# Kernel tuning notes

Hardware: AMD Instinct MI355X
Metric: run time of the kernel (lower is better)

## Reference

```python
import jax, jax.numpy as jnp
import numpy as np

B, T, DIM = 4, 1024, 2048
H, KVH = 16, 4
HD = DIM // H          # 128
G = H // KVH           # GQA group size = 4


def setup_inputs() -> dict:
    key = jax.random.key(0)
    ks = jax.random.split(key, 4)
    s = 1.0 / np.sqrt(DIM)
    x = jax.random.normal(ks[0], (B, T, DIM), jnp.float32)
    Wq = jax.random.normal(ks[1], (DIM, DIM), jnp.float32) * s
    Wkv = jax.random.normal(ks[2], (DIM, 2 * KVH * HD), jnp.float32) * s
    Wo = jax.random.normal(ks[3], (DIM, DIM), jnp.float32) * s
    # RoPE tables (theta=10000, half-split / rotate-half convention)
    inv_freq = 1.0 / (10000.0 ** (np.arange(0, HD, 2, dtype=np.float64) / HD))
    freqs = np.outer(np.arange(T, dtype=np.float64), inv_freq)  # [T, HD/2]
    cos = jnp.asarray(np.cos(freqs), jnp.float32)
    sin = jnp.asarray(np.sin(freqs), jnp.float32)
    return {"x": x, "Wq": Wq, "Wkv": Wkv, "Wo": Wo, "cos": cos, "sin": sin}


def _rope(u, cos, sin):
    # u: [B,T,heads,HD]; cos/sin: [T, HD/2]
    u1, u2 = jnp.split(u, 2, axis=-1)
    c = cos[None, :, None, :]
    s = sin[None, :, None, :]
    return jnp.concatenate([u1 * c - u2 * s, u1 * s + u2 * c], axis=-1)


def reference(x, Wq, Wkv, Wo, cos, sin):
    Bs, Ts, C = x.shape
    q = (x @ Wq).reshape(Bs, Ts, H, HD)
    kv = (x @ Wkv).reshape(Bs, Ts, 2, KVH, HD)
    k, v = kv[:, :, 0], kv[:, :, 1]
    q = _rope(q, cos, sin)
    k = _rope(k, cos, sin)
    # GQA without materializing repeated K/V: fold group dim into q
    qg = q.reshape(Bs, Ts, KVH, G, HD)
    scores = jnp.einsum('bqhgd,bkhd->bhgqk', qg, k) / np.float32(np.sqrt(HD))
    causal = jnp.tril(jnp.ones((Ts, Ts), bool))
    neg = jnp.finfo(scores.dtype).min
    scores = jnp.where(causal, scores, neg)
    att = jax.nn.softmax(scores, axis=-1)
    out = jnp.einsum('bhgqk,bkhd->bqhgd', att, v).reshape(Bs, Ts, C)
    return out @ Wo
```

## Files before the change

kernel.cpp:

```cpp
#include <hip/hip_runtime.h>

typedef unsigned short u16;
typedef unsigned int u32;
typedef __bf16 bf16x8 __attribute__((ext_vector_type(8)));
typedef float f32x4 __attribute__((ext_vector_type(4)));

#define BB   4
#define TT   1024
#define CDIM 2048
#define NH   16
#define NKV  4
#define HDIM 128

__device__ __forceinline__ float b2f(u16 u) {
    union { u32 i; float f; } x; x.i = ((u32)u) << 16; return x.f;
}
__device__ __forceinline__ u16 f2b(float f) {
    union { float f; u32 i; } x; x.f = f;
    u32 r = (x.i + 0x7fffu + ((x.i >> 16) & 1u)) >> 16;
    return (u16)r;
}
__device__ __forceinline__ void async16(const void* g, void* l) {
    __builtin_amdgcn_global_load_lds((const __attribute__((address_space(1))) void*)g,
                                     (__attribute__((address_space(3))) void*)l, 16, 0, 0);
}
template<int N> __device__ __forceinline__ void waitvm() {
    static_assert(N >= 0 && N <= 8, "unsupported vmcnt");
    if constexpr (N == 0)      asm volatile("s_waitcnt vmcnt(0)" ::: "memory");
    else if constexpr (N == 1) asm volatile("s_waitcnt vmcnt(1)" ::: "memory");
    else if constexpr (N == 2) asm volatile("s_waitcnt vmcnt(2)" ::: "memory");
    else if constexpr (N == 3) asm volatile("s_waitcnt vmcnt(3)" ::: "memory");
    else if constexpr (N == 4) asm volatile("s_waitcnt vmcnt(4)" ::: "memory");
    else if constexpr (N == 5) asm volatile("s_waitcnt vmcnt(5)" ::: "memory");
    else if constexpr (N == 6) asm volatile("s_waitcnt vmcnt(6)" ::: "memory");
    else if constexpr (N == 7) asm volatile("s_waitcnt vmcnt(7)" ::: "memory");
    else                       asm volatile("s_waitcnt vmcnt(8)" ::: "memory");
}

__device__ __forceinline__ bool wave_is_f32(const u16* xp) {
    u16 v = xp[(threadIdx.x & 63) * 2];
    int e = (v >> 7) & 0xFF;
    bool bad = (v != 0) && (e < 90 || e > 160);
    return __popcll(__ballot(bad)) > 16;
}

__global__ __launch_bounds__(256) void pre_k(const void* __restrict__ x,
                                             const void* __restrict__ Wq,
                                             const void* __restrict__ Wkv,
                                             const void* __restrict__ Wo,
                                             u16* __restrict__ xb,
                                             u16* __restrict__ csb,
                                             u16* __restrict__ snb,
                                             u16* __restrict__ WqkvT,
                                             u16* __restrict__ WoT,
                                             const void* __restrict__ cs,
                                             const void* __restrict__ sn) {
    const bool f32m = wave_is_f32((const u16*)x);
    int bid = blockIdx.x;
    if (bid < 8320) {
        const void* src; u16* dst; int i;
        if (bid < 8192)      { src = x;  dst = xb;  i = bid * 256 + threadIdx.x; }
        else if (bid < 8256) { src = cs; dst = csb; i = (bid - 8192) * 256 + threadIdx.x; }
        else                 { src = sn; dst = snb; i = (bid - 8256) * 256 + threadIdx.x; }
        union { u16 u[4]; ushort4 v; } o;
        if (f32m) {
            float4 f = ((const float4*)src)[i];
            o.u[0] = f2b(f.x); o.u[1] = f2b(f.y); o.u[2] = f2b(f.z); o.u[3] = f2b(f.w);
        } else {
            o.v = ((const ushort4*)src)[i];
        }
        ((ushort4*)dst)[i] = o.v;
        return;
    }
    __shared__ alignas(16) u16 tile[64 * 65];
    int t = bid - 8320;
    const void* W; u16* WT; int rows, cols, bx, by;
    if (t < 1024)      { W = Wq;  WT = WqkvT;                    rows = 2048; cols = 2048; bx = t & 31;  by = t >> 5; }
    else if (t < 1536) { int l = t - 1024; W = Wkv; WT = WqkvT + (long)2048 * 2048; rows = 2048; cols = 1024; bx = l & 15; by = l >> 4; }
    else               { int l = t - 1536; W = Wo;  WT = WoT;  rows = 2048; cols = 2048; bx = l & 31;   by = l >> 5; }
    const int r0 = by * 64, c0 = bx * 64;
#pragma unroll
    for (int i = 0; i < 16; i++) {
        int c = threadIdx.x + i * 256;
        int rr = c >> 6, cc = c & 63;
        long idx = (long)(r0 + rr) * cols + c0 + cc;
        tile[rr * 65 + cc] = f32m ? f2b(((const float*)W)[idx]) : ((const u16*)W)[idx];
    }
    __syncthreads();
#pragma unroll
    for (int i = 0; i < 16; i++) {
        int c = threadIdx.x + i * 256;
        int rr = c >> 6, cc = c & 63;
        WT[(long)(c0 + rr) * rows + r0 + cc] = tile[cc * 65 + rr];
    }
}

template<int BM, int BN>
__global__ __launch_bounds__(512, 2) void gemm_p4(const u16* __restrict__ A,
                                                  const u16* __restrict__ Bt,
                                                  void* __restrict__ C,
                                                  int N, int Kd,
                                                  const u16* __restrict__ xprobe) {
    constexpr int MF  = BM / 32;
    constexpr int NF  = BN / 64;
    constexpr int MF0 = MF / 2, MF1 = MF - MF0;
    constexpr int NF0 = (NF + 1) / 2, NF1 = NF - NF0;
    constexpr int NAU = BM / 64;
    constexpr int NBU = BN / 64;
    constexpr int NAL = NAU / 2;
    constexpr int NBL = NBU / 2;

    __shared__ alignas(16) u16 As[2][BM * 64];
    __shared__ alignas(16) u16 Bs[2][BN * 64];

    const bool f32m = (xprobe != nullptr) && wave_is_f32(xprobe);
    const int tid = threadIdx.x;
    const int w = tid >> 6, lane = tid & 63;
    const int wm = w >> 2, wn = w & 3;
    const int l16 = lane & 15, quad = lane >> 4;
    const long arow0 = (long)blockIdx.y * BM;
    const long brow0 = (long)blockIdx.x * BN;
    const int NT = Kd >> 6;

    const int srow = tid >> 3, scp = tid & 7;
    const long gst = (long)srow * Kd + ((scp ^ (srow & 7)) << 3);
    const int cst = tid << 3;

    const u16* Ab = A + arow0 * Kd;
    const u16* Bb = Bt + brow0 * Kd;

    auto stageA = [&](int buf, int t, int u0, int u1) {
#pragma unroll
        for (int u = 0; u < NAU; u++)
            if (u >= u0 && u < u1)
                async16(Ab + (long)u * 64 * Kd + t * 64 + gst, &As[buf][u * 4096 + cst]);
    };
    auto stageB = [&](int buf, int t, int u0, int u1) {
#pragma unroll
        for (int u = 0; u < NBU; u++)
            if (u >= u0 && u < u1)
                async16(Bb + (long)u * 64 * Kd + t * 64 + gst, &Bs[buf][u * 4096 + cst]);
    };

    const int R0a = wm * (BM / 2) + l16, sA = R0a & 7;
    const int R0b = wn * (BN / 4) + l16, sB = R0b & 7;
    int aoff[2], boff[2];
    aoff[0] = R0a * 64 + ((quad ^ sA) << 3);
    aoff[1] = R0a * 64 + (((4 + quad) ^ sA) << 3);
    boff[0] = R0b * 64 + ((quad ^ sB) << 3);
    boff[1] = R0b * 64 + (((4 + quad) ^ sB) << 3);

    f32x4 acc[MF][NF];
#pragma unroll
    for (int i = 0; i < MF; i++)
#pragma unroll
        for (int j = 0; j < NF; j++) acc[i][j] = {0.f, 0.f, 0.f, 0.f};

    stageB(0, 0, 0, NBU);
    stageA(0, 0, 0, NAU);
    stageB(1, 1, 0, NBL);
    waitvm<NBL>();
    __builtin_amdgcn_s_barrier();

#pragma unroll 1
    for (int t = 0; t < NT; ++t) {
        const int cur = t & 1, nxt = cur ^ 1;
        const u16* pA = &As[cur][0];
        const u16* pB = &Bs[cur][0];
        bf16x8 afLo[MF0][2], afHi[MF1][2], bfA[NF0][2], bfB[NF1][2];

#pragma unroll
        for (int ks = 0; ks < 2; ks++) {
#pragma unroll
            for (int mt = 0; mt < MF0; mt++)
                afLo[mt][ks] = *(const bf16x8*)&pA[aoff[ks] + mt * 1024];
#pragma unroll
            for (int nt = 0; nt < NF0; nt++)
                bfA[nt][ks] = *(const bf16x8*)&pB[boff[ks] + nt * 1024];
        }
        if (t + 1 < NT) stageB(nxt, t + 1, NBL, NBU);
        __builtin_amdgcn_s_barrier();
        asm volatile("s_waitcnt lgkmcnt(0)" ::: "memory");
        __builtin_amdgcn_sched_barrier(0);
        __builtin_amdgcn_s_setprio(1);
#pragma unroll
        for (int ks = 0; ks < 2; ks++)
#pragma unroll
            for (int mt = 0; mt < MF0; mt++)
#pragma unroll
                for (int nt = 0; nt < NF0; nt++)
                    acc[mt][nt] = __builtin_amdgcn_mfma_f32_16x16x32_bf16(
                        afLo[mt][ks], bfA[nt][ks], acc[mt][nt], 0, 0, 0);
        __builtin_amdgcn_s_setprio(0);

#pragma unroll
        for (int ks = 0; ks < 2; ks++)
#pragma unroll
            for (int nt = 0; nt < NF1; nt++)
                bfB[nt][ks] = *(const bf16x8*)&pB[boff[ks] + (NF0 + nt) * 1024];
        if (t + 1 < NT) stageA(nxt, t + 1, 0, NAL);
        __builtin_amdgcn_s_barrier();
        asm volatile("s_waitcnt lgkmcnt(0)" ::: "memory");
        __builtin_amdgcn_sched_barrier(0);
        __builtin_amdgcn_s_setprio(1);
#pragma unroll
        for (int ks = 0; ks < 2; ks++)
#pragma unroll
            for (int mt = 0; mt < MF0; mt++)
#pragma unroll
                for (int nt = 0; nt < NF1; nt++)
                    acc[mt][NF0 + nt] = __builtin_amdgcn_mfma_f32_16x16x32_bf16(
                        afLo[mt][ks], bfB[nt][ks], acc[mt][NF0 + nt], 0, 0, 0);
        __builtin_amdgcn_s_setprio(0);

#pragma unroll
        for (int ks = 0; ks < 2; ks++)
#pragma unroll
            for (int mt = 0; mt < MF1; mt++)
                afHi[mt][ks] = *(const bf16x8*)&pA[aoff[ks] + (MF0 + mt) * 1024];
        if (t + 1 < NT) stageA(nxt, t + 1, NAL, NAU);
        __builtin_amdgcn_s_barrier();
        asm volatile("s_waitcnt lgkmcnt(0)" ::: "memory");
        __builtin_amdgcn_sched_barrier(0);
        __builtin_amdgcn_s_setprio(1);
#pragma unroll
        for (int ks = 0; ks < 2; ks++)
#pragma unroll
            for (int mt = 0; mt < MF1; mt++)
#pragma unroll
                for (int nt = 0; nt < NF1; nt++)
                    acc[MF0 + mt][NF0 + nt] = __builtin_amdgcn_mfma_f32_16x16x32_bf16(
                        afHi[mt][ks], bfB[nt][ks], acc[MF0 + mt][NF0 + nt], 0, 0, 0);
        __builtin_amdgcn_s_setprio(0);

        if (t + 1 < NT) {
            asm volatile("s_waitcnt vmcnt(0)" ::: "memory");
            __builtin_amdgcn_s_barrier();
            if (t + 2 < NT) stageB(cur, t + 2, 0, NBL);
        }
        __builtin_amdgcn_sched_barrier(0);
        __builtin_amdgcn_s_setprio(1);
#pragma unroll
        for (int ks = 0; ks < 2; ks++)
#pragma unroll
            for (int mt = 0; mt < MF1; mt++)
#pragma unroll
                for (int nt = 0; nt < NF0; nt++)
                    acc[MF0 + mt][nt] = __builtin_amdgcn_mfma_f32_16x16x32_bf16(
                        afHi[mt][ks], bfA[nt][ks], acc[MF0 + mt][nt], 0, 0, 0);
        __builtin_amdgcn_s_setprio(0);
    }

#pragma unroll
    for (int mt = 0; mt < MF; mt++) {
#pragma unroll
        for (int nt = 0; nt < NF; nt++) {
            long col = brow0 + wn * (BN / 4) + nt * 16 + l16;
#pragma unroll
            for (int r = 0; r < 4; r++) {
                long row = arow0 + wm * (BM / 2) + mt * 16 + quad * 4 + r;
                if (f32m) ((float*)C)[row * N + col] = acc[mt][nt][r];
                else      ((u16*)C)[row * N + col] = f2b(acc[mt][nt][r]);
            }
        }
    }
}

template<int BM, int BN>
__global__ __launch_bounds__(512, 2) void gemm_p2(const u16* __restrict__ A,
                                                  const u16* __restrict__ Bt,
                                                  void* __restrict__ C,
                                                  int N, int Kd,
                                                  const u16* __restrict__ xprobe) {
    constexpr int MF  = BM / 32;
    constexpr int NF  = BN / 64;
    constexpr int MF0 = MF / 2, MF1 = MF - MF0;
    constexpr int NF0 = (NF + 1) / 2, NF1 = NF - NF0;
    constexpr int NAU = BM / 64;
    constexpr int NBU = BN / 64;

    __shared__ alignas(16) u16 As[2][BM * 64];
    __shared__ alignas(16) u16 Bs[2][BN * 64];

    const bool f32m = (xprobe != nullptr) && wave_is_f32(xprobe);
    const int tid = threadIdx.x;
    const int w = tid >> 6, lane = tid & 63;
    const int wm = w >> 2, wn = w & 3;
    const int l16 = lane & 15, quad = lane >> 4;
    const long arow0 = (long)blockIdx.y * BM;
    const long brow0 = (long)blockIdx.x * BN;
    const int NT = Kd >> 6;

    const int srow = tid >> 3, scp = tid & 7;
    const long gst = (long)srow * Kd + ((scp ^ (srow & 7)) << 3);
    const int cst = tid << 3;

    const u16* Ab = A + arow0 * Kd;
    const u16* Bb = Bt + brow0 * Kd;

    auto stageA = [&](int buf, int t) {
#pragma unroll
        for (int u = 0; u < NAU; u++)
            async16(Ab + (long)u * 64 * Kd + t * 64 + gst, &As[buf][u * 4096 + cst]);
    };
    auto stageB = [&](int buf, int t) {
#pragma unroll
        for (int u = 0; u < NBU; u++)
            async16(Bb + (long)u * 64 * Kd + t * 64 + gst, &Bs[buf][u * 4096 + cst]);
    };

    const int R0a = wm * (BM / 2) + l16, sA = R0a & 7;
    const int R0b = wn * (BN / 4) + l16, sB = R0b & 7;
    int aoff[2], boff[2];
    aoff[0] = R0a * 64 + ((quad ^ sA) << 3);
    aoff[1] = R0a * 64 + (((4 + quad) ^ sA) << 3);
    boff[0] = R0b * 64 + ((quad ^ sB) << 3);
    boff[1] = R0b * 64 + (((4 + quad) ^ sB) << 3);

    f32x4 acc[MF][NF];
#pragma unroll
    for (int i = 0; i < MF; i++)
#pragma unroll
        for (int j = 0; j < NF; j++) acc[i][j] = {0.f, 0.f, 0.f, 0.f};

    stageB(0, 0); stageA(0, 0); stageB(1, 1); stageA(1, 1);
    waitvm<NAU + NBU>();
    __builtin_amdgcn_s_barrier();

#pragma unroll 1
    for (int t = 0; t < NT; ++t) {
        const int cur = t & 1;
        const u16* pA = &As[cur][0];
        const u16* pB = &Bs[cur][0];
        bf16x8 afLo[MF0][2], afHi[MF1][2], bfA[NF0][2], bfB[NF1][2];

#pragma unroll
        for (int ks = 0; ks < 2; ks++) {
#pragma unroll
            for (int mt = 0; mt < MF0; mt++)
                afLo[mt][ks] = *(const bf16x8*)&pA[aoff[ks] + mt * 1024];
#pragma unroll
            for (int nt = 0; nt < NF0; nt++)
                bfA[nt][ks] = *(const bf16x8*)&pB[boff[ks] + nt * 1024];
#pragma unroll
            for (int nt = 0; nt < NF1; nt++)
                bfB[nt][ks] = *(const bf16x8*)&pB[boff[ks] + (NF0 + nt) * 1024];
        }
        asm volatile("s_waitcnt lgkmcnt(0)" ::: "memory");
        __builtin_amdgcn_sched_barrier(0);
        __builtin_amdgcn_s_setprio(1);
#pragma unroll
        for (int ks = 0; ks < 2; ks++)
#pragma unroll
            for (int mt = 0; mt < MF0; mt++) {
#pragma unroll
                for (int nt = 0; nt < NF0; nt++)
                    acc[mt][nt] = __builtin_amdgcn_mfma_f32_16x16x32_bf16(
                        afLo[mt][ks], bfA[nt][ks], acc[mt][nt], 0, 0, 0);
#pragma unroll
                for (int nt = 0; nt < NF1; nt++)
                    acc[mt][NF0 + nt] = __builtin_amdgcn_mfma_f32_16x16x32_bf16(
                        afLo[mt][ks], bfB[nt][ks], acc[mt][NF0 + nt], 0, 0, 0);
            }
        __builtin_amdgcn_s_setprio(0);

#pragma unroll
        for (int ks = 0; ks < 2; ks++)
#pragma unroll
            for (int mt = 0; mt < MF1; mt++)
                afHi[mt][ks] = *(const bf16x8*)&pA[aoff[ks] + (MF0 + mt) * 1024];
        __builtin_amdgcn_s_barrier();
        if (t + 2 < NT) stageB(cur, t + 2);
        asm volatile("s_waitcnt lgkmcnt(0)" ::: "memory");
        __builtin_amdgcn_sched_barrier(0);
        __builtin_amdgcn_s_setprio(1);
#pragma unroll
        for (int ks = 0; ks < 2; ks++)
#pragma unroll
            for (int mt = 0; mt < MF1; mt++) {
#pragma unroll
                for (int nt = 0; nt < NF1; nt++)
                    acc[MF0 + mt][NF0 + nt] = __builtin_amdgcn_mfma_f32_16x16x32_bf16(
                        afHi[mt][ks], bfB[nt][ks], acc[MF0 + mt][NF0 + nt], 0, 0, 0);
#pragma unroll
                for (int nt = 0; nt < NF0; nt++)
                    acc[MF0 + mt][nt] = __builtin_amdgcn_mfma_f32_16x16x32_bf16(
                        afHi[mt][ks], bfA[nt][ks], acc[MF0 + mt][nt], 0, 0, 0);
            }
        __builtin_amdgcn_s_setprio(0);

        if (t + 1 < NT) {
            if (t + 2 < NT) waitvm<NBU>();
            else            waitvm<0>();
            __builtin_amdgcn_s_barrier();
            if (t + 2 < NT) stageA(cur, t + 2);
        }
    }

#pragma unroll
    for (int mt = 0; mt < MF; mt++) {
#pragma unroll
        for (int nt = 0; nt < NF; nt++) {
            long col = brow0 + wn * (BN / 4) + nt * 16 + l16;
#pragma unroll
            for (int r = 0; r < 4; r++) {
                long row = arow0 + wm * (BM / 2) + mt * 16 + quad * 4 + r;
                if (f32m) ((float*)C)[row * N + col] = acc[mt][nt][r];
                else      ((u16*)C)[row * N + col] = f2b(acc[mt][nt][r]);
            }
        }
    }
}

__global__ __launch_bounds__(256) void prep_k(const u16* __restrict__ QKVraw,
                                              const u16* __restrict__ cs,
                                              const u16* __restrict__ sn,
                                              u16* __restrict__ Qr,
                                              u16* __restrict__ Kr,
                                              u16* __restrict__ Vt) {
    __shared__ alignas(16) u16 tile[64 * 68];
    int bid = blockIdx.x;
    if (bid < 16384) {
        int idx = bid * 256 + threadIdx.x;
        int d = idx & 63;
        int t = (idx >> 6) & (TT - 1);
        int bh = idx >> 16;
        long src = ((long)((bh >> 4) * TT + t)) * 3072 + (bh & 15) * HDIM;
        float u1 = b2f(QKVraw[src + d]), u2 = b2f(QKVraw[src + d + 64]);
        float c = b2f(cs[t * 64 + d]), s = b2f(sn[t * 64 + d]);
        long dst = ((long)bh * TT + t) * HDIM;
        Qr[dst + d] = f2b(u1 * c - u2 * s);
        Qr[dst + d + 64] = f2b(u1 * s + u2 * c);
    } else if (bid < 20480) {
        int idx = (bid - 16384) * 256 + threadIdx.x;
        int d = idx & 63;
        int t = (idx >> 6) & (TT - 1);
        int bk = idx >> 16;
        long src = ((long)((bk >> 2) * TT + t)) * 3072 + 2048 + (bk & 3) * HDIM;
        float u1 = b2f(QKVraw[src + d]), u2 = b2f(QKVraw[src + d + 64]);
        float c = b2f(cs[t * 64 + d]), s = b2f(sn[t * 64 + d]);
        long dst = ((long)bk * TT + t) * HDIM;
        Kr[dst + d] = f2b(u1 * c - u2 * s);
        Kr[dst + d + 64] = f2b(u1 * s + u2 * c);
    } else {
        int vb = bid - 20480;
        int bk = vb >> 5;
        int dt = (vb >> 4) & 1;
        int tt = vb & 15;
        const int d0 = dt * 64, t0 = tt * 64;
        const long srcb = ((long)(bk >> 2) * TT) * 3072 + 2560 + (bk & 3) * HDIM;
#pragma unroll
        for (int i = 0; i < 4; i++) {
            int lin = i * 256 + threadIdx.x;
            int r = lin >> 4, c4 = (lin & 15) * 4;
            *(ushort4*)&tile[r * 68 + c4] =
                *(const ushort4*)&QKVraw[srcb + (long)(t0 + r) * 3072 + d0 + c4];
        }
        __syncthreads();
        const long dstb = ((long)bk * 128 + d0) * 1024 + t0;
#pragma unroll
        for (int i = 0; i < 4; i++) {
            int lin = i * 256 + threadIdx.x;
            int dr = lin >> 4, c4 = (lin & 15) * 4;
            ushort4 v;
            v.x = tile[(c4 + 0) * 68 + dr];
            v.y = tile[(c4 + 1) * 68 + dr];
            v.z = tile[(c4 + 2) * 68 + dr];
            v.w = tile[(c4 + 3) * 68 + dr];
            *(ushort4*)&Vt[dstb + (long)dr * 1024 + c4] = v;
        }
    }
}

__global__ __launch_bounds__(256) void attn_kernel(const u16* __restrict__ Q,
                                                   const u16* __restrict__ Kr,
                                                   const u16* __restrict__ Vt,
                                                   u16* __restrict__ O) {
    __shared__ alignas(16) u16 Ks[2][64 * 128];
    __shared__ alignas(16) u16 Vts[2][128 * 64];
    __shared__ alignas(16) u16 Ps[64 * 88];

    const int tid = threadIdx.x, w = tid >> 6, lane = tid & 63;
    const int l16 = lane & 15, quad = lane >> 4;
    const float scale2 = 0.08838834764831845f * 1.4426950408889634f;

#pragma unroll 1
    for (int it = 0; it < 2; it++) {
        const int j = it ? (1023 - (int)blockIdx.x) : (int)blockIdx.x;
        const int qt = 15 - (j >> 6);
        const int bh = j & 63;
        const int b = bh >> 4, h = bh & 15;
        const int kvh = h >> 2;
        const long qrow0 = (long)bh * TT + qt * 64;
        const long krow0 = (long)(b * NKV + kvh) * TT;
        const long vbase = ((long)(b * NKV + kvh) * HDIM) * TT;

        __syncthreads();

#pragma unroll
        for (int i = 0; i < 4; i++) {
            int slot0 = (w * 4 + i) * 64;
            int slot = slot0 + lane;
            int row = slot >> 4, cp = slot & 15;
            int cg = (cp & 8) | ((cp ^ row) & 7);
            async16(Q + (qrow0 + row) * HDIM + cg * 8, &Ks[0][slot0 * 8]);
        }
        asm volatile("s_waitcnt vmcnt(0)" ::: "memory");
        bf16x8 qf[4];
        {
            const int Rq = w * 16 + l16;
#pragma unroll
            for (int ds = 0; ds < 4; ds++) {
                int c = ds * 4 + quad;
                qf[ds] = *(const bf16x8*)&Ks[0][Rq * 128 + ((c & 8) | ((c ^ Rq) & 7)) * 8];
            }
        }
        asm volatile("s_waitcnt lgkmcnt(0)" ::: "memory");

#pragma unroll
        for (int i = 0; i < 4; i++) {
            int slot0 = (w * 4 + i) * 64;
            int slot = slot0 + lane;
            int row = slot >> 4, cp = slot & 15;
            int cg = (cp & 8) | ((cp ^ row) & 7);
            async16(Kr + (krow0 + row) * HDIM + cg * 8, &Ks[0][slot0 * 8]);
        }
#pragma unroll
        for (int i = 0; i < 4; i++) {
            int slot0 = (w * 4 + i) * 64;
            int slot = slot0 + lane;
            int row = slot >> 3, cp = slot & 7;
            int cg = cp ^ (row & 7);
            async16(Vt + vbase + (long)row * TT + cg * 8, &Vts[0][slot0 * 8]);
        }
        if (qt >= 1) {
#pragma unroll
            for (int i = 0; i < 4; i++) {
                int slot0 = (w * 4 + i) * 64;
                int slot = slot0 + lane;
                int row = slot >> 4, cp = slot & 15;
                int cg = (cp & 8) | ((cp ^ row) & 7);
                async16(Kr + (krow0 + 64 + row) * HDIM + cg * 8, &Ks[1][slot0 * 8]);
            }
#pragma unroll
            for (int i = 0; i < 4; i++) {
                int slot0 = (w * 4 + i) * 64;
                int slot = slot0 + lane;
                int row = slot >> 3, cp = slot & 7;
                int cg = cp ^ (row & 7);
                async16(Vt + vbase + (long)row * TT + 64 + cg * 8, &Vts[1][slot0 * 8]);
            }
            asm volatile("s_waitcnt vmcnt(8)" ::: "memory");
        } else {
            asm volatile("s_waitcnt vmcnt(0)" ::: "memory");
        }
        asm volatile("s_barrier" ::: "memory");

        f32x4 o[8];
#pragma unroll
        for (int i = 0; i < 8; i++) o[i] = {0.f, 0.f, 0.f, 0.f};
        float m_i = -1.0e30f, l_i = 0.f;
        const int qg = qt * 64 + w * 16 + l16;

#pragma unroll 1
        for (int kt = 0; kt <= qt; kt++) {
            const int cur = kt & 1;
            const u16* ksb = Ks[cur];
            const u16* vsb = Vts[cur];

            f32x4 s[4];
#pragma unroll
            for (int nt = 0; nt < 4; nt++) s[nt] = {0.f, 0.f, 0.f, 0.f};
#pragma unroll
            for (int ds = 0; ds < 4; ds++) {
                int c = ds * 4 + quad;
#pragma unroll
                for (int nt = 0; nt < 4; nt++) {
                    int Rk = nt * 16 + l16;
                    bf16x8 ak = *(const bf16x8*)&ksb[Rk * 128 + ((c & 8) | ((c ^ Rk) & 7)) * 8];
                    s[nt] = __builtin_amdgcn_mfma_f32_16x16x32_bf16(ak, qf[ds], s[nt], 0, 0, 0);
                }
            }

            float p[4][4];
            float mx = -1.0e30f;
            if (kt == qt) {
#pragma unroll
                for (int nt = 0; nt < 4; nt++)
#pragma unroll
                    for (int r = 0; r < 4; r++) {
                        int kcol = kt * 64 + nt * 16 + quad * 4 + r;
                        float v = (kcol <= qg) ? (float)s[nt][r] * scale2 : -1.0e30f;
                        p[nt][r] = v;
                        mx = fmaxf(mx, v);
                    }
            } else {
#pragma unroll
                for (int nt = 0; nt < 4; nt++)
#pragma unroll
                    for (int r = 0; r < 4; r++) {
                        float v = (float)s[nt][r] * scale2;
                        p[nt][r] = v;
                        mx = fmaxf(mx, v);
                    }
            }
            mx = fmaxf(mx, __shfl_xor(mx, 16));
            mx = fmaxf(mx, __shfl_xor(mx, 32));
            float mnew = fmaxf(m_i, mx);
            float alpha = exp2f(m_i - mnew);
            float rs = 0.f;
#pragma unroll
            for (int nt = 0; nt < 4; nt++)
#pragma unroll
                for (int r = 0; r < 4; r++) {
                    float e = exp2f(p[nt][r] - mnew);
                    p[nt][r] = e;
                    rs += e;
                }
            rs += __shfl_xor(rs, 16);
            rs += __shfl_xor(rs, 32);
            l_i = l_i * alpha + rs;

            u32* Psw = (u32*)Ps;
            int pb = (w * 16 + l16) * 44 + quad * 2;
#pragma unroll
            for (int nt = 0; nt < 4; nt++) {
                u32 lo = (u32)f2b(p[nt][0]) | ((u32)f2b(p[nt][1]) << 16);
                u32 hi = (u32)f2b(p[nt][2]) | ((u32)f2b(p[nt][3]) << 16);
                Psw[pb + nt * 8]     = lo;
                Psw[pb + nt * 8 + 1] = hi;
            }
            if (__ballot(mnew != m_i) != 0ULL) {
#pragma unroll
                for (int n8 = 0; n8 < 8; n8++)
#pragma unroll
                    for (int r = 0; r < 4; r++) o[n8][r] *= alpha;
            }
            m_i = mnew;

            asm volatile("s_waitcnt lgkmcnt(0)" ::: "memory");

#pragma unroll
            for (int ks = 0; ks < 2; ks++) {
                bf16x8 bp = *(const bf16x8*)&Ps[(w * 16 + l16) * 88 + ks * 32 + quad * 8];
#pragma unroll
                for (int n8 = 0; n8 < 8; n8++) {
                    int Rv = n8 * 16 + l16;
                    int c = ks * 4 + quad;
                    bf16x8 av = *(const bf16x8*)&vsb[Rv * 64 + (c ^ (Rv & 7)) * 8];
                    o[n8] = __builtin_amdgcn_mfma_f32_16x16x32_bf16(av, bp, o[n8], 0, 0, 0);
                }
            }

            if (kt == qt) break;

            asm volatile("s_waitcnt lgkmcnt(0)" ::: "memory");
            asm volatile("s_barrier" ::: "memory");
            if (kt + 2 <= qt) {
                const int nk = kt + 2;
#pragma unroll
                for (int i = 0; i < 4; i++) {
                    int slot0 = (w * 4 + i) * 64;
                    int slot = slot0 + lane;
                    int row = slot >> 4, cp = slot & 15;
                    int cg = (cp & 8) | ((cp ^ row) & 7);
                    async16(Kr + (krow0 + nk * 64 + row) * HDIM + cg * 8, &Ks[cur][slot0 * 8]);
                }
#pragma unroll
                for (int i = 0; i < 4; i++) {
                    int slot0 = (w * 4 + i) * 64;
                    int slot = slot0 + lane;
                    int row = slot >> 3, cp = slot & 7;
                    int cg = cp ^ (row & 7);
                    async16(Vt + vbase + (long)row * TT + nk * 64 + cg * 8, &Vts[cur][slot0 * 8]);
                }
                asm volatile("s_waitcnt vmcnt(8)" ::: "memory");
            } else {
                asm volatile("s_waitcnt vmcnt(0)" ::: "memory");
            }
            asm volatile("s_barrier" ::: "memory");
        }

        float inv = 1.0f / l_i;
        long obase = ((long)(b * TT + qg)) * CDIM + h * HDIM;
#pragma unroll
        for (int n8 = 0; n8 < 8; n8++) {
            ushort4 st;
            st.x = f2b(o[n8][0] * inv);
            st.y = f2b(o[n8][1] * inv);
            st.z = f2b(o[n8][2] * inv);
            st.w = f2b(o[n8][3] * inv);
            *(ushort4*)&O[obase + n8 * 16 + quad * 4] = st;
        }
    }
}

extern "C" void kernel_launch(void* const* d_in, const int* in_sizes, int n_in,
                              void* d_out, int out_size, void* d_ws, size_t ws_size,
                              hipStream_t stream) {
    const void* x   = d_in[0];
    const void* Wq  = d_in[1];
    const void* Wkv = d_in[2];
    const void* Wo  = d_in[3];
    const void* cs  = d_in[4];
    const void* sn  = d_in[5];

    char* ws = (char*)d_ws;
    const size_t NEED = 105119748;
    if (ws_size < NEED) return;

    u16* WqkvT = (u16*)(ws + 0);
    u16* WoT   = (u16*)(ws + 12582912);
    u16* QKVraw= (u16*)(ws + 20971520);
    u16* Qr    = (u16*)(ws + 46137344);
    u16* Kr    = (u16*)(ws + 62914560);
    u16* Vt    = (u16*)(ws + 67108864);
    u16* ATT   = (u16*)(ws + 71303168);
    u16* xb    = (u16*)(ws + 88080384);
    u16* csb   = (u16*)(ws + 104857600);
    u16* snb   = (u16*)(ws + 104988672);

    pre_k<<<10880, 256, 0, stream>>>(x, Wq, Wkv, Wo, xb, csb, snb, WqkvT, WoT, cs, sn);

    gemm_p4<256, 192><<<dim3(16, 16), 512, 0, stream>>>(xb, WqkvT, QKVraw, 3072, 2048, nullptr);

    prep_k<<<20992, 256, 0, stream>>>(QKVraw, csb, snb, Qr, Kr, Vt);

    attn_kernel<<<512, 256, 0, stream>>>(Qr, Kr, Vt, ATT);

    gemm_p2<128, 256><<<dim3(8, 32), 512, 0, stream>>>(ATT, WoT, d_out, 2048, 2048, (const u16*)x);
}
```

Baseline: 299.5 us.

## Shrink GEMM tiles, raise occupancy bounds, and prioritize attention MFMA phases

```diff
diff --git a/kernel.cpp b/kernel.cpp
--- a/kernel.cpp
+++ b/kernel.cpp
@@ -96,7 +96,7 @@
 }
 
 template<int BM, int BN>
-__global__ __launch_bounds__(512, 2) void gemm_p4(const u16* __restrict__ A,
+__global__ __launch_bounds__(512, 4) void gemm_p4(const u16* __restrict__ A,
                                                   const u16* __restrict__ Bt,
                                                   void* __restrict__ C,
                                                   int N, int Kd,
@@ -267,7 +267,7 @@
 }
 
 template<int BM, int BN>
-__global__ __launch_bounds__(512, 2) void gemm_p2(const u16* __restrict__ A,
+__global__ __launch_bounds__(512, 4) void gemm_p2(const u16* __restrict__ A,
                                                   const u16* __restrict__ Bt,
                                                   void* __restrict__ C,
                                                   int N, int Kd,
@@ -571,6 +571,7 @@
             f32x4 s[4];
 #pragma unroll
             for (int nt = 0; nt < 4; nt++) s[nt] = {0.f, 0.f, 0.f, 0.f};
+            __builtin_amdgcn_s_setprio(1);
 #pragma unroll
             for (int ds = 0; ds < 4; ds++) {
                 int c = ds * 4 + quad;
@@ -581,42 +582,42 @@
                     s[nt] = __builtin_amdgcn_mfma_f32_16x16x32_bf16(ak, qf[ds], s[nt], 0, 0, 0);
                 }
             }
+            __builtin_amdgcn_s_setprio(0);
 
             float p[4][4];
-            float mx = -1.0e30f;
             if (kt == qt) {
 #pragma unroll
                 for (int nt = 0; nt < 4; nt++)
 #pragma unroll
                     for (int r = 0; r < 4; r++) {
                         int kcol = kt * 64 + nt * 16 + quad * 4 + r;
-                        float v = (kcol <= qg) ? (float)s[nt][r] * scale2 : -1.0e30f;
-                        p[nt][r] = v;
-                        mx = fmaxf(mx, v);
+                        p[nt][r] = (kcol <= qg) ? (float)s[nt][r] * scale2 : -1.0e30f;
                     }
             } else {
 #pragma unroll
                 for (int nt = 0; nt < 4; nt++)
 #pragma unroll
-                    for (int r = 0; r < 4; r++) {
-                        float v = (float)s[nt][r] * scale2;
-                        p[nt][r] = v;
-                        mx = fmaxf(mx, v);
-                    }
-            }
+                    for (int r = 0; r < 4; r++)
+                        p[nt][r] = (float)s[nt][r] * scale2;
+            }
+            float mrow[4];
+#pragma unroll
+            for (int nt = 0; nt < 4; nt++)
+                mrow[nt] = fmaxf(fmaxf(p[nt][0], p[nt][1]), fmaxf(p[nt][2], p[nt][3]));
+            float mx = fmaxf(fmaxf(mrow[0], mrow[1]), fmaxf(mrow[2], mrow[3]));
             mx = fmaxf(mx, __shfl_xor(mx, 16));
             mx = fmaxf(mx, __shfl_xor(mx, 32));
             float mnew = fmaxf(m_i, mx);
             float alpha = exp2f(m_i - mnew);
-            float rs = 0.f;
-#pragma unroll
-            for (int nt = 0; nt < 4; nt++)
-#pragma unroll
-                for (int r = 0; r < 4; r++) {
-                    float e = exp2f(p[nt][r] - mnew);
-                    p[nt][r] = e;
-                    rs += e;
-                }
+            float rrow[4];
+#pragma unroll
+            for (int nt = 0; nt < 4; nt++) {
+#pragma unroll
+                for (int r = 0; r < 4; r++)
+                    p[nt][r] = exp2f(p[nt][r] - mnew);
+                rrow[nt] = (p[nt][0] + p[nt][1]) + (p[nt][2] + p[nt][3]);
+            }
+            float rs = (rrow[0] + rrow[1]) + (rrow[2] + rrow[3]);
             rs += __shfl_xor(rs, 16);
             rs += __shfl_xor(rs, 32);
             l_i = l_i * alpha + rs;
@@ -640,6 +641,7 @@
 
             asm volatile("s_waitcnt lgkmcnt(0)" ::: "memory");
 
+            __builtin_amdgcn_s_setprio(1);
 #pragma unroll
             for (int ks = 0; ks < 2; ks++) {
                 bf16x8 bp = *(const bf16x8*)&Ps[(w * 16 + l16) * 88 + ks * 32 + quad * 8];
@@ -651,6 +653,7 @@
                     o[n8] = __builtin_amdgcn_mfma_f32_16x16x32_bf16(av, bp, o[n8], 0, 0, 0);
                 }
             }
+            __builtin_amdgcn_s_setprio(0);
 
             if (kt == qt) break;
 
@@ -722,11 +725,11 @@
 
     pre_k<<<10880, 256, 0, stream>>>(x, Wq, Wkv, Wo, xb, csb, snb, WqkvT, WoT, cs, sn);
 
-    gemm_p4<256, 192><<<dim3(16, 16), 512, 0, stream>>>(xb, WqkvT, QKVraw, 3072, 2048, nullptr);
+    gemm_p4<128, 192><<<dim3(16, 32), 512, 0, stream>>>(xb, WqkvT, QKVraw, 3072, 2048, nullptr);
 
     prep_k<<<20992, 256, 0, stream>>>(QKVraw, csb, snb, Qr, Kr, Vt);
 
     attn_kernel<<<512, 256, 0, stream>>>(Qr, Kr, Vt, ATT);
 
-    gemm_p2<128, 256><<<dim3(8, 32), 512, 0, stream>>>(ATT, WoT, d_out, 2048, 2048, (const u16*)x);
-}
+    gemm_p2<128, 128><<<dim3(16, 32), 512, 0, stream>>>(ATT, WoT, d_out, 2048, 2048, (const u16*)x);
+}
```

Result: faster. 287.2 us (-4.1%).
